# Optimization experiments

Hardware: AMD Instinct MI355X
Metric: run time of the kernel (lower is better)

Reference implementation:

```python
import jax, jax.numpy as jnp
import numpy as np

B, S, D, M, H, HD, V = 256, 128, 512, 150, 8, 64, 10000
LN_EPS = 1e-5

def layer_norm(x, g, b):
    mu = jnp.mean(x, axis=-1, keepdims=True)
    var = jnp.mean((x - mu) ** 2, axis=-1, keepdims=True)
    return (x - mu) * jax.lax.rsqrt(var + LN_EPS) * g + b

def setup_inputs() -> dict:
    key = jax.random.key(0)
    ks = jax.random.split(key, 20)
    s = 0.02
    return {
        'x': jax.random.randint(ks[0], (B, S), 0, V),
        'emb': jax.random.normal(ks[1], (V, D)) * s,
        'W1': jax.random.normal(ks[2], (M, D, D)) * s,   # [mode, out, in]
        'b1': jnp.zeros((M, D)),
        'ln1_g': jnp.ones((M, D)),
        'ln1_b': jnp.zeros((M, D)),
        'W2': jax.random.normal(ks[3], (M, D, D)) * s,
        'b2': jnp.zeros((M, D)),
        'dbias': jax.random.normal(ks[4], (M, D)) * 0.01,
        'in_proj_w': jax.random.normal(ks[5], (3 * D, D)) * s,
        'in_proj_b': jnp.zeros((3 * D,)),
        'out_proj_w': jax.random.normal(ks[6], (D, D)) * s,
        'out_proj_b': jnp.zeros((D,)),
        'norm_g': jnp.ones((D,)),
        'norm_b': jnp.zeros((D,)),
        'dec_w1': jax.random.normal(ks[7], (D // 2, D)) * s,
        'dec_b1': jnp.zeros((D // 2,)),
        'dec_w2': jax.random.normal(ks[8], (V, D // 2)) * s,
        'dec_b2': jnp.zeros((V,)),
    }

def reference(x, emb, W1, b1, ln1_g, ln1_b, W2, b2, dbias,
              in_proj_w, in_proj_b, out_proj_w, out_proj_b,
              norm_g, norm_b, dec_w1, dec_b1, dec_w2, dec_b2):
    # shared embedding: [B,S] -> [B,D]
    e = jnp.take(emb, x, axis=0).mean(axis=1)
    # 150 mode heads as grouped GEMMs: Linear -> LN -> ReLU -> Linear + bias
    h = jnp.einsum('bd,mod->bmo', e, W1) + b1                    # [B,M,D]
    h = layer_norm(h, ln1_g, ln1_b)
    h = jax.nn.relu(h)                                            # dropout = identity (eval)
    mode_out = jnp.einsum('bmd,mod->bmo', h, W2) + b2 + dbias     # [B,M,D]
    # cross-mode self-attention (torch MultiheadAttention, batch_first)
    qkv = mode_out @ in_proj_w.T + in_proj_b                      # [B,M,3D]
    q, k, v = jnp.split(qkv, 3, axis=-1)
    q = q.reshape(B, M, H, HD); k = k.reshape(B, M, H, HD); v = v.reshape(B, M, H, HD)
    scores = jnp.einsum('bqhd,bkhd->bhqk', q, k) / np.sqrt(HD)
    attn = jax.nn.softmax(scores, axis=-1)
    o = jnp.einsum('bhqk,bkhd->bqhd', attn, v).reshape(B, M, D)
    attended = o @ out_proj_w.T + out_proj_b                      # [B,M,D]
    # gating mask: active_modes=None -> all ones, so gated == attended
    agg = layer_norm(attended.sum(axis=1), norm_g, norm_b)        # [B,D]
    # decoder: Linear -> ReLU -> Linear
    dec = jax.nn.relu(agg @ dec_w1.T + dec_b1)
    return dec @ dec_w2.T + dec_b2                                # [B,V]
```

## Files before the change

kernel.cpp:

```cpp
#include <hip/hip_runtime.h>

typedef __attribute__((ext_vector_type(8))) short s16x8;
typedef __attribute__((ext_vector_type(8))) unsigned short u16x8;
typedef __attribute__((ext_vector_type(4))) float f32x4;

#define LN_EPS 1e-5f

__device__ inline float bf2f(unsigned short u) {
    union { unsigned int i; float f; } x; x.i = ((unsigned int)u) << 16; return x.f;
}
__device__ inline unsigned short f2bf(float f) {
    unsigned int u = __builtin_bit_cast(unsigned int, f);
    u += 0x7FFFu + ((u >> 16) & 1u);
    return (unsigned short)(u >> 16);
}
__device__ inline unsigned int cvt_pk_bf16(float lo, float hi) {
    unsigned int r;
    asm("v_cvt_pk_bf16_f32 %0, %1, %2" : "=v"(r) : "v"(lo), "v"(hi));
    return r;
}
typedef __attribute__((address_space(1))) const unsigned int as1_u32;
typedef __attribute__((address_space(3))) unsigned int as3_u32;
__device__ inline void gl2lds16(const void* g, void* l) {
    __builtin_amdgcn_global_load_lds((as1_u32*)g, (as3_u32*)l, 16, 0, 0);
}

__global__ __launch_bounds__(256) void cvt_bf16_kernel(
    const float* __restrict__ in, unsigned short* __restrict__ out, int n8)
{
    int i = blockIdx.x * 256 + threadIdx.x;
    const int stride = gridDim.x * 256;
    for (; i < n8; i += stride) {
        const float4 a = ((const float4*)in)[2 * i];
        const float4 b = ((const float4*)in)[2 * i + 1];
        union { unsigned int u[4]; u16x8 v; } r;
        r.u[0] = cvt_pk_bf16(a.x, a.y);
        r.u[1] = cvt_pk_bf16(a.z, a.w);
        r.u[2] = cvt_pk_bf16(b.x, b.y);
        r.u[3] = cvt_pk_bf16(b.z, b.w);
        ((u16x8*)out)[i] = r.v;
    }
}

template<int K, bool RELU, bool F32OUT>
__global__ __launch_bounds__(256, 4) void gemm_bf_kernel(
    const unsigned short* __restrict__ A,
    const unsigned short* __restrict__ Wb,
    const float* __restrict__ bias1,
    const float* __restrict__ bias2,
    float bias_scale,
    void* __restrict__ Cv,
    int N, int gx, int gy,
    size_t strideA_mode, size_t lda,
    size_t strideW_mode, size_t strideB_mode,
    size_t strideC_mode, size_t ldc)
{
    constexpr int NSTEP = K / 32;

    const int nwg = gridDim.x, wgid = blockIdx.x;
    const int q8 = nwg >> 3, r8 = nwg & 7;
    const int xcd = wgid & 7, sub = wgid >> 3;
    int p = (xcd < r8 ? xcd * (q8 + 1) : r8 * (q8 + 1) + (xcd - r8) * q8) + sub;
    const int bx = p % gx; p /= gx;
    const int by = p % gy;
    const int bz = p / gy;
    const int n0 = bx * 128, r0 = by * 128;

    __shared__ __align__(16) unsigned char lds[2][16384];

    const int tid = threadIdx.x, lane = tid & 63, wid = tid >> 6;
    const int fr = lane & 15, ks = lane >> 4;
    const int wr = (wid >> 1) * 64, wc = (wid & 1) * 64;

    const int Ia0 = (wid * 2 + 0) * 64 + lane;
    const int Ia1 = (wid * 2 + 1) * 64 + lane;
    const int ar0 = Ia0 >> 2, ac0 = (Ia0 & 3) ^ (ar0 & 3);
    const int ar1 = Ia1 >> 2, ac1 = (Ia1 & 3) ^ (ar1 & 3);
    const unsigned char* Aslab = (const unsigned char*)(A + (size_t)bz * strideA_mode);
    const unsigned char* aSrc0 = Aslab + (size_t)(r0 + ar0) * lda * 2 + ac0 * 16;
    const unsigned char* aSrc1 = Aslab + (size_t)(r0 + ar1) * lda * 2 + ac1 * 16;
    const unsigned char* Wslab = (const unsigned char*)(Wb + (size_t)bz * strideW_mode);
    const int br0 = min(n0 + ar0, N - 1), br1 = min(n0 + ar1, N - 1);
    const unsigned char* bSrc0 = Wslab + (size_t)br0 * K * 2 + ac0 * 16;
    const unsigned char* bSrc1 = Wslab + (size_t)br1 * K * 2 + ac1 * 16;

    f32x4 acc[4][4];
#pragma unroll
    for (int i = 0; i < 4; ++i)
#pragma unroll
        for (int j = 0; j < 4; ++j)
#pragma unroll
            for (int r = 0; r < 4; ++r) acc[i][j][r] = 0.f;

    auto stage = [&](int buf, int t) {
        gl2lds16(aSrc0 + (size_t)t * 64, &lds[buf][(wid * 2 + 0) * 1024]);
        gl2lds16(aSrc1 + (size_t)t * 64, &lds[buf][(wid * 2 + 1) * 1024]);
        gl2lds16(bSrc0 + (size_t)t * 64, &lds[buf][8192 + (wid * 2 + 0) * 1024]);
        gl2lds16(bSrc1 + (size_t)t * 64, &lds[buf][8192 + (wid * 2 + 1) * 1024]);
    };

    auto compute = [&](int buf) {
        const unsigned char* Ab = &lds[buf][0];
        const unsigned char* Bb = &lds[buf][8192];
        const int co = (ks ^ (fr & 3)) << 4;
        s16x8 af[4], bfr[4];
#pragma unroll
        for (int mi = 0; mi < 4; ++mi)
            af[mi] = *(const s16x8*)(Ab + (wr + mi * 16 + fr) * 64 + co);
#pragma unroll
        for (int ni = 0; ni < 4; ++ni)
            bfr[ni] = *(const s16x8*)(Bb + (wc + ni * 16 + fr) * 64 + co);
#pragma unroll
        for (int mi = 0; mi < 4; ++mi)
#pragma unroll
            for (int ni = 0; ni < 4; ++ni)
                acc[mi][ni] = __builtin_amdgcn_mfma_f32_16x16x32_bf16(af[mi], bfr[ni], acc[mi][ni], 0, 0, 0);
    };

    stage(0, 0);
    __syncthreads();

    for (int t = 0; t < NSTEP; t += 2) {
        stage(1, t + 1);
        compute(0);
        __syncthreads();
        if (t + 2 < NSTEP) stage(0, t + 2);
        compute(1);
        __syncthreads();
    }

    if (!F32OUT) {
        unsigned short* Cl = (unsigned short*)&lds[0][0];
#pragma unroll
        for (int ni = 0; ni < 4; ++ni) {
            const int col = n0 + wc + ni * 16 + fr;
            float bsum = 0.f;
            if (bias1) bsum += bias_scale * bias1[(size_t)bz * strideB_mode + col];
            if (bias2) bsum += bias2[(size_t)bz * strideB_mode + col];
#pragma unroll
            for (int mi = 0; mi < 4; ++mi)
#pragma unroll
                for (int r = 0; r < 4; ++r) {
                    float v = acc[mi][ni][r] + bsum;
                    if (RELU) v = fmaxf(v, 0.f);
                    Cl[(wr + mi * 16 + ks * 4 + r) * 128 + wc + ni * 16 + fr] = f2bf(v);
                }
        }
        __syncthreads();
        unsigned short* Cg = (unsigned short*)Cv + (size_t)bz * strideC_mode;
#pragma unroll
        for (int it = 0; it < 8; ++it) {
            const int c = it * 256 + tid;
            const int row = c >> 4, ch = c & 15;
            u16x8 v = *(const u16x8*)(&Cl[row * 128 + ch * 8]);
            *(u16x8*)(Cg + (size_t)(r0 + row) * ldc + n0 + ch * 8) = v;
        }
    } else {
#pragma unroll
        for (int ni = 0; ni < 4; ++ni) {
            const int col = n0 + wc + ni * 16 + fr;
            if (col < N) {
                float bsum = 0.f;
                if (bias1) bsum += bias_scale * bias1[(size_t)bz * strideB_mode + col];
                if (bias2) bsum += bias2[(size_t)bz * strideB_mode + col];
#pragma unroll
                for (int mi = 0; mi < 4; ++mi)
#pragma unroll
                    for (int r = 0; r < 4; ++r) {
                        const int row = r0 + wr + mi * 16 + ks * 4 + r;
                        float v = acc[mi][ni][r] + bsum;
                        if (RELU) v = fmaxf(v, 0.f);
                        ((float*)Cv)[(size_t)bz * strideC_mode + (size_t)row * ldc + col] = v;
                    }
            }
        }
    }
}

__global__ __launch_bounds__(512) void embed_kernel(
    const int* __restrict__ x, const float* __restrict__ emb,
    unsigned short* __restrict__ e)
{
    const int b = blockIdx.x;
    __shared__ int xs[128];
    const int tid = threadIdx.x;
    if (tid < 128) xs[tid] = x[b * 128 + tid];
    __syncthreads();
    float s = 0.f;
    for (int i = 0; i < 128; ++i) s += emb[(size_t)xs[i] * 512 + tid];
    e[(size_t)b * 512 + tid] = f2bf(s * (1.f / 128.f));
}

template<bool RELU>
__global__ __launch_bounds__(256) void ln_kernel(
    const unsigned short* __restrict__ X,
    const float* __restrict__ G,
    const float* __restrict__ Bt,
    unsigned short* __restrict__ Y,
    int M)
{
    const int row = blockIdx.x;
    const int m = row % M;
    const unsigned short* xr = X + (size_t)row * 512;
    unsigned short* yr = Y + (size_t)row * 512;
    const int tid = threadIdx.x;
    const float x0 = bf2f(xr[tid]), x1 = bf2f(xr[tid + 256]);
    float s = x0 + x1, q = x0 * x0 + x1 * x1;
#pragma unroll
    for (int off = 32; off; off >>= 1) {
        s += __shfl_xor(s, off);
        q += __shfl_xor(q, off);
    }
    __shared__ float red[4][2];
    const int wid = tid >> 6, lane = tid & 63;
    if (lane == 0) { red[wid][0] = s; red[wid][1] = q; }
    __syncthreads();
    s = red[0][0] + red[1][0] + red[2][0] + red[3][0];
    q = red[0][1] + red[1][1] + red[2][1] + red[3][1];
    const float mu = s * (1.f / 512.f);
    const float var = q * (1.f / 512.f) - mu * mu;
    const float rstd = rsqrtf(var + LN_EPS);
    const float* g = G + (size_t)m * 512;
    const float* bt = Bt + (size_t)m * 512;
    float y0 = (x0 - mu) * rstd * g[tid] + bt[tid];
    float y1 = (x1 - mu) * rstd * g[tid + 256] + bt[tid + 256];
    if (RELU) { y0 = fmaxf(y0, 0.f); y1 = fmaxf(y1, 0.f); }
    yr[tid] = f2bf(y0);
    yr[tid + 256] = f2bf(y1);
}

#define KP 72
#define VP 168
__global__ __launch_bounds__(256) void attn_mfma_kernel(
    const unsigned short* __restrict__ qkv, unsigned short* __restrict__ o_att,
    int b0)
{
    const int bl = blockIdx.x >> 3, h = blockIdx.x & 7;
    __shared__ __align__(16) unsigned short k_s[160 * KP];
    __shared__ __align__(16) unsigned short v_t[64 * VP];
    __shared__ __align__(16) unsigned short p_s[4][16 * VP];
    const int tid = threadIdx.x, lane = tid & 63, wid = tid >> 6;
    const int fr = lane & 15, ks = lane >> 4;
    const size_t base = (size_t)bl * (150 * 1536) + h * 64;

    for (int idx = tid; idx < 160 * 8; idx += 256) {
        const int r = idx >> 3, c8 = (idx & 7) * 8;
        u16x8 v;
        if (r < 150) v = *(const u16x8*)(qkv + base + (size_t)r * 1536 + 512 + c8);
        else {
#pragma unroll
            for (int j = 0; j < 8; ++j) v[j] = 0;
        }
        *(u16x8*)(&k_s[r * KP + c8]) = v;
    }
    for (int idx = tid; idx < 160 * 8; idx += 256) {
        const int c8 = idx / 160, r = idx - c8 * 160;
        u16x8 v;
        if (r < 150) v = *(const u16x8*)(qkv + base + (size_t)r * 1536 + 1024 + c8 * 8);
        else {
#pragma unroll
            for (int j = 0; j < 8; ++j) v[j] = 0;
        }
#pragma unroll
        for (int j = 0; j < 8; ++j) v_t[(c8 * 8 + j) * VP + r] = v[j];
    }
    __syncthreads();

    unsigned short* pw = &p_s[wid][0];

    for (int qt = wid; qt < 10; qt += 4) {
        const int qr = (qt * 16 + fr < 150) ? qt * 16 + fr : 149;
        const unsigned short* qp = qkv + base + (size_t)qr * 1536;
        s16x8 qa0 = *(const s16x8*)(qp + ks * 8);
        s16x8 qa1 = *(const s16x8*)(qp + 32 + ks * 8);

        f32x4 acc[10];
#pragma unroll
        for (int t = 0; t < 10; ++t)
#pragma unroll
            for (int r = 0; r < 4; ++r) acc[t][r] = 0.f;
#pragma unroll
        for (int t = 0; t < 10; ++t) {
            s16x8 kb0 = *(const s16x8*)(&k_s[(t * 16 + fr) * KP + ks * 8]);
            s16x8 kb1 = *(const s16x8*)(&k_s[(t * 16 + fr) * KP + 32 + ks * 8]);
            acc[t] = __builtin_amdgcn_mfma_f32_16x16x32_bf16(qa0, kb0, acc[t], 0, 0, 0);
            acc[t] = __builtin_amdgcn_mfma_f32_16x16x32_bf16(qa1, kb1, acc[t], 0, 0, 0);
        }

        const bool v9 = (fr < 6);
        float inv[4];
#pragma unroll
        for (int i = 0; i < 4; ++i) {
            float m = -1e30f;
#pragma unroll
            for (int t = 0; t < 9; ++t) m = fmaxf(m, acc[t][i]);
            if (v9) m = fmaxf(m, acc[9][i]);
#pragma unroll
            for (int off = 1; off < 16; off <<= 1) m = fmaxf(m, __shfl_xor(m, off));
            float s = 0.f;
#pragma unroll
            for (int t = 0; t < 10; ++t) {
                float e = 0.f;
                if (t < 9 || v9) e = __expf(0.125f * (acc[t][i] - m));
                s += e;
                pw[(ks * 4 + i) * VP + t * 16 + fr] = f2bf(e);
            }
#pragma unroll
            for (int off = 1; off < 16; off <<= 1) s += __shfl_xor(s, off);
            inv[i] = 1.f / s;
        }

        f32x4 o[4];
#pragma unroll
        for (int dt = 0; dt < 4; ++dt)
#pragma unroll
            for (int r = 0; r < 4; ++r) o[dt][r] = 0.f;
#pragma unroll
        for (int kc = 0; kc < 5; ++kc) {
            s16x8 pa = *(const s16x8*)(&pw[fr * VP + kc * 32 + ks * 8]);
#pragma unroll
            for (int dt = 0; dt < 4; ++dt) {
                s16x8 vb = *(const s16x8*)(&v_t[(dt * 16 + fr) * VP + kc * 32 + ks * 8]);
                o[dt] = __builtin_amdgcn_mfma_f32_16x16x32_bf16(pa, vb, o[dt], 0, 0, 0);
            }
        }

#pragma unroll
        for (int dt = 0; dt < 4; ++dt) {
            const int d = h * 64 + dt * 16 + fr;
#pragma unroll
            for (int i = 0; i < 4; ++i) {
                const int q = qt * 16 + ks * 4 + i;
                if (q < 150)
                    o_att[((size_t)((b0 + bl) * 150 + q)) * 512 + d] = f2bf(o[dt][i] * inv[i]);
            }
        }
    }
}

__global__ __launch_bounds__(512) void osum_kernel(
    const unsigned short* __restrict__ o_att, unsigned short* __restrict__ osum)
{
    const int b = blockIdx.x, tid = threadIdx.x;
    float s = 0.f;
    const unsigned short* p = o_att + (size_t)b * 150 * 512 + tid;
    for (int mm = 0; mm < 150; ++mm) s += bf2f(p[(size_t)mm * 512]);
    osum[(size_t)b * 512 + tid] = f2bf(s);
}

extern "C" void kernel_launch(void* const* d_in, const int* in_sizes, int n_in,
                              void* d_out, int out_size, void* d_ws, size_t ws_size,
                              hipStream_t stream)
{
    (void)in_sizes; (void)n_in; (void)out_size; (void)ws_size;

    const int*   x          = (const int*)d_in[0];
    const float* emb        = (const float*)d_in[1];
    const float* W1         = (const float*)d_in[2];
    const float* b1         = (const float*)d_in[3];
    const float* ln1_g      = (const float*)d_in[4];
    const float* ln1_b      = (const float*)d_in[5];
    const float* W2         = (const float*)d_in[6];
    const float* b2         = (const float*)d_in[7];
    const float* dbias      = (const float*)d_in[8];
    const float* in_proj_w  = (const float*)d_in[9];
    const float* in_proj_b  = (const float*)d_in[10];
    const float* out_proj_w = (const float*)d_in[11];
    const float* out_proj_b = (const float*)d_in[12];
    const float* norm_g     = (const float*)d_in[13];
    const float* norm_b     = (const float*)d_in[14];
    const float* dec_w1     = (const float*)d_in[15];
    const float* dec_b1     = (const float*)d_in[16];
    const float* dec_w2     = (const float*)d_in[17];
    const float* dec_b2     = (const float*)d_in[18];

    char* ws = (char*)d_ws;
    unsigned short* e_bf  = (unsigned short*)(ws + 0x0);
    unsigned short* osum  = (unsigned short*)(ws + 0x40000);
    unsigned short* att1  = (unsigned short*)(ws + 0x80000);
    unsigned short* agg   = (unsigned short*)(ws + 0xC0000);
    unsigned short* dec1  = (unsigned short*)(ws + 0x100000);
    unsigned short* h1    = (unsigned short*)(ws + 0x200000);
    unsigned short* mo    = (unsigned short*)(ws + 0x2800000);
    unsigned short* qkvb  = (unsigned short*)(ws + 0x4E00000);
    unsigned short* Wbf   = (unsigned short*)(ws + 0x6B00000);
    unsigned short* ipwbf = (unsigned short*)(ws + 0xB600000);
    unsigned short* opwbf = (unsigned short*)(ws + 0xB780000);
    unsigned short* dw1bf = (unsigned short*)(ws + 0xB800000);
    unsigned short* dw2bf = (unsigned short*)(ws + 0xB840000);
    unsigned short* o_att = h1;

    embed_kernel<<<256, 512, 0, stream>>>(x, emb, e_bf);

    cvt_bf16_kernel<<<384, 256, 0, stream>>>(in_proj_w, ipwbf, 1536 * 512 / 8);
    cvt_bf16_kernel<<<128, 256, 0, stream>>>(out_proj_w, opwbf, 512 * 512 / 8);
    cvt_bf16_kernel<<<64, 256, 0, stream>>>(dec_w1, dw1bf, 256 * 512 / 8);
    cvt_bf16_kernel<<<1280, 256, 0, stream>>>(dec_w2, dw2bf, 10000 * 256 / 8);

    cvt_bf16_kernel<<<2048, 256, 0, stream>>>(W1, Wbf, 150 * 512 * 512 / 8);

    gemm_bf_kernel<512, false, false><<<4 * 2 * 150, 256, 0, stream>>>(
        e_bf, Wbf, b1, nullptr, 1.f, h1,
        512, 4, 2,
        (size_t)0, 512, (size_t)512 * 512, 512, 512, 76800);

    ln_kernel<true><<<38400, 256, 0, stream>>>(h1, ln1_g, ln1_b, h1, 150);

    cvt_bf16_kernel<<<2048, 256, 0, stream>>>(W2, Wbf, 150 * 512 * 512 / 8);

    gemm_bf_kernel<512, false, false><<<4 * 2 * 150, 256, 0, stream>>>(
        h1, Wbf, b2, dbias, 1.f, mo,
        512, 4, 2,
        (size_t)512, 76800, (size_t)512 * 512, 512, 512, 76800);

    for (int c = 0; c < 4; ++c) {
        gemm_bf_kernel<512, false, false><<<12 * 75, 256, 0, stream>>>(
            mo + (size_t)c * 64 * 76800, ipwbf, in_proj_b, nullptr, 1.f, qkvb,
            1536, 12, 75,
            (size_t)0, 512, (size_t)0, 0, 0, 1536);
        attn_mfma_kernel<<<512, 256, 0, stream>>>(qkvb, o_att, c * 64);
    }

    osum_kernel<<<256, 512, 0, stream>>>(o_att, osum);

    gemm_bf_kernel<512, false, false><<<4 * 2, 256, 0, stream>>>(
        osum, opwbf, out_proj_b, nullptr, 150.f, att1,
        512, 4, 2,
        (size_t)0, 512, (size_t)0, 0, 0, 512);

    ln_kernel<false><<<256, 256, 0, stream>>>(att1, norm_g, norm_b, agg, 1);

    gemm_bf_kernel<512, true, false><<<2 * 2, 256, 0, stream>>>(
        agg, dw1bf, dec_b1, nullptr, 1.f, dec1,
        256, 2, 2,
        (size_t)0, 512, (size_t)0, 0, 0, 256);

    gemm_bf_kernel<256, false, true><<<79 * 2, 256, 0, stream>>>(
        dec1, dw2bf, dec_b2, nullptr, 1.f, d_out,
        10000, 79, 2,
        (size_t)0, 256, (size_t)0, 0, 0, 10000);
}
```

Before: 419.1 us.

## Fuse prep launches, overlap W2 conversion with GEMM1, unchunk QKV and attention

Result: faster. 397.7 us (-5.1%).

```diff
diff --git a/kernel.cpp b/kernel.cpp
--- a/kernel.cpp
+++ b/kernel.cpp
@@ -25,22 +25,60 @@
     __builtin_amdgcn_global_load_lds((as1_u32*)g, (as3_u32*)l, 16, 0, 0);
 }
 
-__global__ __launch_bounds__(256) void cvt_bf16_kernel(
-    const float* __restrict__ in, unsigned short* __restrict__ out, int n8)
-{
-    int i = blockIdx.x * 256 + threadIdx.x;
-    const int stride = gridDim.x * 256;
+__device__ inline void cvt_stream(const float* __restrict__ src,
+                                  unsigned short* __restrict__ dst,
+                                  int n8, int lb, int nb, int tid)
+{
+    int i = lb * 256 + tid;
+    const int stride = nb * 256;
     for (; i < n8; i += stride) {
-        const float4 a = ((const float4*)in)[2 * i];
-        const float4 b = ((const float4*)in)[2 * i + 1];
+        const float4 a = ((const float4*)src)[2 * i];
+        const float4 b = ((const float4*)src)[2 * i + 1];
         union { unsigned int u[4]; u16x8 v; } r;
         r.u[0] = cvt_pk_bf16(a.x, a.y);
         r.u[1] = cvt_pk_bf16(a.z, a.w);
         r.u[2] = cvt_pk_bf16(b.x, b.y);
         r.u[3] = cvt_pk_bf16(b.z, b.w);
-        ((u16x8*)out)[i] = r.v;
-    }
-}
+        ((u16x8*)dst)[i] = r.v;
+    }
+}
+
+__global__ __launch_bounds__(256) void prep_kernel(
+    const int* __restrict__ x, const float* __restrict__ emb,
+    unsigned short* __restrict__ e,
+    const float* __restrict__ w1, unsigned short* __restrict__ w1b,
+    const float* __restrict__ ipw, unsigned short* __restrict__ ipwb,
+    const float* __restrict__ opw, unsigned short* __restrict__ opwb,
+    const float* __restrict__ dw1, unsigned short* __restrict__ dw1b,
+    const float* __restrict__ dw2, unsigned short* __restrict__ dw2b)
+{
+    const int tid = threadIdx.x;
+    int b = blockIdx.x;
+    if (b < 256) {
+        __shared__ int xs[128];
+        if (tid < 128) xs[tid] = x[b * 128 + tid];
+        __syncthreads();
+        float s0 = 0.f, s1 = 0.f;
+        for (int i = 0; i < 128; ++i) {
+            const float* r = emb + (size_t)xs[i] * 512;
+            s0 += r[tid]; s1 += r[tid + 256];
+        }
+        e[(size_t)b * 512 + tid] = f2bf(s0 * (1.f / 128.f));
+        e[(size_t)b * 512 + tid + 256] = f2bf(s1 * (1.f / 128.f));
+        return;
+    }
+    b -= 256;
+    if (b < 2048) { cvt_stream(w1, w1b, 150 * 512 * 512 / 8, b, 2048, tid); return; }
+    b -= 2048;
+    if (b < 384) { cvt_stream(ipw, ipwb, 1536 * 512 / 8, b, 384, tid); return; }
+    b -= 384;
+    if (b < 128) { cvt_stream(opw, opwb, 512 * 512 / 8, b, 128, tid); return; }
+    b -= 128;
+    if (b < 64) { cvt_stream(dw1, dw1b, 256 * 512 / 8, b, 64, tid); return; }
+    b -= 64;
+    cvt_stream(dw2, dw2b, 10000 * 256 / 8, b, 1280, tid);
+}
+#define PREP_BLOCKS (256 + 2048 + 384 + 128 + 64 + 1280)
 
 template<int K, bool RELU, bool F32OUT>
 __global__ __launch_bounds__(256, 4) void gemm_bf_kernel(
@@ -50,15 +88,23 @@
     const float* __restrict__ bias2,
     float bias_scale,
     void* __restrict__ Cv,
-    int N, int gx, int gy,
+    int N, int gx, int gy, int ngemm,
     size_t strideA_mode, size_t lda,
     size_t strideW_mode, size_t strideB_mode,
-    size_t strideC_mode, size_t ldc)
+    size_t strideC_mode, size_t ldc,
+    const float* __restrict__ cvt_src, unsigned short* __restrict__ cvt_dst,
+    int cvt_n8)
 {
     constexpr int NSTEP = K / 32;
-
-    const int nwg = gridDim.x, wgid = blockIdx.x;
-    const int q8 = nwg >> 3, r8 = nwg & 7;
+    const int tid = threadIdx.x;
+    const int wgid = blockIdx.x;
+
+    if (wgid >= ngemm) {
+        cvt_stream(cvt_src, cvt_dst, cvt_n8, wgid - ngemm, gridDim.x - ngemm, tid);
+        return;
+    }
+
+    const int q8 = ngemm >> 3, r8 = ngemm & 7;
     const int xcd = wgid & 7, sub = wgid >> 3;
     int p = (xcd < r8 ? xcd * (q8 + 1) : r8 * (q8 + 1) + (xcd - r8) * q8) + sub;
     const int bx = p % gx; p /= gx;
@@ -68,7 +114,7 @@
 
     __shared__ __align__(16) unsigned char lds[2][16384];
 
-    const int tid = threadIdx.x, lane = tid & 63, wid = tid >> 6;
+    const int lane = tid & 63, wid = tid >> 6;
     const int fr = lane & 15, ks = lane >> 4;
     const int wr = (wid >> 1) * 64, wc = (wid & 1) * 64;
 
@@ -175,20 +221,6 @@
             }
         }
     }
-}
-
-__global__ __launch_bounds__(512) void embed_kernel(
-    const int* __restrict__ x, const float* __restrict__ emb,
-    unsigned short* __restrict__ e)
-{
-    const int b = blockIdx.x;
-    __shared__ int xs[128];
-    const int tid = threadIdx.x;
-    if (tid < 128) xs[tid] = x[b * 128 + tid];
-    __syncthreads();
-    float s = 0.f;
-    for (int i = 0; i < 128; ++i) s += emb[(size_t)xs[i] * 512 + tid];
-    e[(size_t)b * 512 + tid] = f2bf(s * (1.f / 128.f));
 }
 
 template<bool RELU>
@@ -232,16 +264,15 @@
 #define KP 72
 #define VP 168
 __global__ __launch_bounds__(256) void attn_mfma_kernel(
-    const unsigned short* __restrict__ qkv, unsigned short* __restrict__ o_att,
-    int b0)
-{
-    const int bl = blockIdx.x >> 3, h = blockIdx.x & 7;
+    const unsigned short* __restrict__ qkv, unsigned short* __restrict__ o_att)
+{
+    const int b = blockIdx.x >> 3, h = blockIdx.x & 7;
     __shared__ __align__(16) unsigned short k_s[160 * KP];
     __shared__ __align__(16) unsigned short v_t[64 * VP];
     __shared__ __align__(16) unsigned short p_s[4][16 * VP];
     const int tid = threadIdx.x, lane = tid & 63, wid = tid >> 6;
     const int fr = lane & 15, ks = lane >> 4;
-    const size_t base = (size_t)bl * (150 * 1536) + h * 64;
+    const size_t base = (size_t)b * (150 * 1536) + h * 64;
 
     for (int idx = tid; idx < 160 * 8; idx += 256) {
         const int r = idx >> 3, c8 = (idx & 7) * 8;
@@ -332,7 +363,7 @@
             for (int i = 0; i < 4; ++i) {
                 const int q = qt * 16 + ks * 4 + i;
                 if (q < 150)
-                    o_att[((size_t)((b0 + bl) * 150 + q)) * 512 + d] = f2bf(o[dt][i] * inv[i]);
+                    o_att[((size_t)(b * 150 + q)) * 512 + d] = f2bf(o[dt][i] * inv[i]);
             }
         }
     }
@@ -382,61 +413,60 @@
     unsigned short* dec1  = (unsigned short*)(ws + 0x100000);
     unsigned short* h1    = (unsigned short*)(ws + 0x200000);
     unsigned short* mo    = (unsigned short*)(ws + 0x2800000);
-    unsigned short* qkvb  = (unsigned short*)(ws + 0x4E00000);
-    unsigned short* Wbf   = (unsigned short*)(ws + 0x6B00000);
-    unsigned short* ipwbf = (unsigned short*)(ws + 0xB600000);
-    unsigned short* opwbf = (unsigned short*)(ws + 0xB780000);
-    unsigned short* dw1bf = (unsigned short*)(ws + 0xB800000);
-    unsigned short* dw2bf = (unsigned short*)(ws + 0xB840000);
+    unsigned short* qkvf  = (unsigned short*)(ws + 0x4E00000);
+    unsigned short* Wbf1  = (unsigned short*)(ws + 0xBE80000);
+    unsigned short* Wbf2  = (unsigned short*)(ws + 0x10980000);
+    unsigned short* ipwbf = (unsigned short*)(ws + 0x15480000);
+    unsigned short* opwbf = (unsigned short*)(ws + 0x15600000);
+    unsigned short* dw1bf = (unsigned short*)(ws + 0x15700000);
+    unsigned short* dw2bf = (unsigned short*)(ws + 0x15800000);
     unsigned short* o_att = h1;
 
-    embed_kernel<<<256, 512, 0, stream>>>(x, emb, e_bf);
-
-    cvt_bf16_kernel<<<384, 256, 0, stream>>>(in_proj_w, ipwbf, 1536 * 512 / 8);
-    cvt_bf16_kernel<<<128, 256, 0, stream>>>(out_proj_w, opwbf, 512 * 512 / 8);
-    cvt_bf16_kernel<<<64, 256, 0, stream>>>(dec_w1, dw1bf, 256 * 512 / 8);
-    cvt_bf16_kernel<<<1280, 256, 0, stream>>>(dec_w2, dw2bf, 10000 * 256 / 8);
-
-    cvt_bf16_kernel<<<2048, 256, 0, stream>>>(W1, Wbf, 150 * 512 * 512 / 8);
-
-    gemm_bf_kernel<512, false, false><<<4 * 2 * 150, 256, 0, stream>>>(
-        e_bf, Wbf, b1, nullptr, 1.f, h1,
-        512, 4, 2,
-        (size_t)0, 512, (size_t)512 * 512, 512, 512, 76800);
+    prep_kernel<<<PREP_BLOCKS, 256, 0, stream>>>(
+        x, emb, e_bf, W1, Wbf1, in_proj_w, ipwbf, out_proj_w, opwbf,
+        dec_w1, dw1bf, dec_w2, dw2bf);
+
+    gemm_bf_kernel<512, false, false><<<1200 + 2048, 256, 0, stream>>>(
+        e_bf, Wbf1, b1, nullptr, 1.f, h1,
+        512, 4, 2, 1200,
+        (size_t)0, 512, (size_t)512 * 512, 512, 512, 76800,
+        W2, Wbf2, 150 * 512 * 512 / 8);
 
     ln_kernel<true><<<38400, 256, 0, stream>>>(h1, ln1_g, ln1_b, h1, 150);
 
-    cvt_bf16_kernel<<<2048, 256, 0, stream>>>(W2, Wbf, 150 * 512 * 512 / 8);
-
-    gemm_bf_kernel<512, false, false><<<4 * 2 * 150, 256, 0, stream>>>(
-        h1, Wbf, b2, dbias, 1.f, mo,
-        512, 4, 2,
-        (size_t)512, 76800, (size_t)512 * 512, 512, 512, 76800);
-
-    for (int c = 0; c < 4; ++c) {
-        gemm_bf_kernel<512, false, false><<<12 * 75, 256, 0, stream>>>(
-            mo + (size_t)c * 64 * 76800, ipwbf, in_proj_b, nullptr, 1.f, qkvb,
-            1536, 12, 75,
-            (size_t)0, 512, (size_t)0, 0, 0, 1536);
-        attn_mfma_kernel<<<512, 256, 0, stream>>>(qkvb, o_att, c * 64);
-    }
+    gemm_bf_kernel<512, false, false><<<1200, 256, 0, stream>>>(
+        h1, Wbf2, b2, dbias, 1.f, mo,
+        512, 4, 2, 1200,
+        (size_t)512, 76800, (size_t)512 * 512, 512, 512, 76800,
+        nullptr, nullptr, 0);
+
+    gemm_bf_kernel<512, false, false><<<3600, 256, 0, stream>>>(
+        mo, ipwbf, in_proj_b, nullptr, 1.f, qkvf,
+        1536, 12, 300, 3600,
+        (size_t)0, 512, (size_t)0, 0, 0, 1536,
+        nullptr, nullptr, 0);
+
+    attn_mfma_kernel<<<2048, 256, 0, stream>>>(qkvf, o_att);
 
     osum_kernel<<<256, 512, 0, stream>>>(o_att, osum);
 
-    gemm_bf_kernel<512, false, false><<<4 * 2, 256, 0, stream>>>(
+    gemm_bf_kernel<512, false, false><<<8, 256, 0, stream>>>(
         osum, opwbf, out_proj_b, nullptr, 150.f, att1,
-        512, 4, 2,
-        (size_t)0, 512, (size_t)0, 0, 0, 512);
+        512, 4, 2, 8,
+        (size_t)0, 512, (size_t)0, 0, 0, 512,
+        nullptr, nullptr, 0);
 
     ln_kernel<false><<<256, 256, 0, stream>>>(att1, norm_g, norm_b, agg, 1);
 
-    gemm_bf_kernel<512, true, false><<<2 * 2, 256, 0, stream>>>(
+    gemm_bf_kernel<512, true, false><<<4, 256, 0, stream>>>(
         agg, dw1bf, dec_b1, nullptr, 1.f, dec1,
-        256, 2, 2,
-        (size_t)0, 512, (size_t)0, 0, 0, 256);
-
-    gemm_bf_kernel<256, false, true><<<79 * 2, 256, 0, stream>>>(
+        256, 2, 2, 4,
+        (size_t)0, 512, (size_t)0, 0, 0, 256,
+        nullptr, nullptr, 0);
+
+    gemm_bf_kernel<256, false, true><<<158, 256, 0, stream>>>(
         dec1, dw2bf, dec_b2, nullptr, 1.f, d_out,
-        10000, 79, 2,
-        (size_t)0, 256, (size_t)0, 0, 0, 10000);
-}
+        10000, 79, 2, 158,
+        (size_t)0, 256, (size_t)0, 0, 0, 10000,
+        nullptr, nullptr, 0);
+}
```
